# Kernel optimization log

Measured on AMD Instinct MI355X. Metric: run time of the kernel, lower is better.

Reference implementation:

```python
import jax, jax.numpy as jnp
import numpy as np

PAD = 4  # kernel 9, 'same' padding

def _conv1d(x, w):
    # x: [B, C, L], w: [O, I, K] -> [B, O, L] (same padding)
    return jax.lax.conv_general_dilated(x, w, (1,), [(PAD, PAD)],
                                        dimension_numbers=("NCW", "OIW", "NCW"))

def _sweep(x, w, b, axis, reverse):
    # Sequential SCNN sweep along `axis`: slice_i = relu(conv1d(slice_i) + b + slice_{i-1})
    xs = jnp.moveaxis(x, axis, 0)  # [L, B, C, K_len]
    if reverse:
        xs = xs[::-1]
    def step(carry, row):
        y = jax.nn.relu(_conv1d(row, w) + b[None, :, None] + carry)
        return y, y
    _, outs = jax.lax.scan(step, xs[0], xs[1:])
    res = jnp.concatenate([xs[:1], outs], axis=0)
    if reverse:
        res = res[::-1]
    return jnp.moveaxis(res, 0, axis)

def setup_inputs() -> dict:
    key = jax.random.key(0)
    ks = jax.random.split(key, 9)
    B, C, H, W, K = 16, 64, 128, 256, 9
    scale = 1.0 / np.sqrt(C * K).astype(np.float32)
    inp = {"x": jax.random.normal(ks[0], (B, C, H, W), jnp.float32)}
    for i, n in enumerate(["ud", "du", "lr", "rl"]):
        inp[f"w_{n}"] = jax.random.normal(ks[1 + 2 * i], (C, C, K), jnp.float32) * scale
        inp[f"b_{n}"] = jax.random.normal(ks[2 + 2 * i], (C,), jnp.float32) * scale
    return inp

def reference(x, w_ud, b_ud, w_du, b_du, w_lr, b_lr, w_rl, b_rl):
    # down sweep over rows (conv along width), then up sweep
    x = _sweep(x, w_ud, b_ud, axis=2, reverse=False)
    x = _sweep(x, w_du, b_du, axis=2, reverse=True)
    # left->right sweep over columns (conv along height), then right->left
    x = _sweep(x, w_lr, b_lr, axis=3, reverse=False)
    x = _sweep(x, w_rl, b_rl, axis=3, reverse=True)
    return x
```

## Files before the change

kernel.cpp:

```cpp
#include <hip/hip_runtime.h>

#define B_ 16
#define C_ 64
#define H_ 128
#define W_ 256
#define K_ 9
#define KDIM_ (K_*C_)

typedef __attribute__((ext_vector_type(8))) short short8_t;
typedef __attribute__((ext_vector_type(4))) float f32x4;

static __device__ __forceinline__ float bf2f(unsigned short u) {
  union { unsigned int i; float f; } v; v.i = ((unsigned int)u) << 16; return v.f;
}
static __device__ __forceinline__ unsigned short f2bf(float f) {
  union { float f; unsigned int i; } v; v.f = f;
  unsigned int r = v.i + 0x7FFF + ((v.i >> 16) & 1);
  return (unsigned short)(r >> 16);
}

static __device__ __forceinline__ void gload_lds16(const void* g, void* l) {
  __builtin_amdgcn_global_load_lds(
      (const __attribute__((address_space(1))) unsigned int*)g,
      (__attribute__((address_space(3))) unsigned int*)l, 16, 0, 0);
}

__global__ __launch_bounds__(256) void prep_w_all(const float* __restrict__ w0,
                                                  const float* __restrict__ w1,
                                                  const float* __restrict__ w2,
                                                  const float* __restrict__ w3,
                                                  unsigned short* __restrict__ A2,
                                                  float* __restrict__ ZPf) {
  if (blockIdx.y == 0 && blockIdx.x == 0) ZPf[threadIdx.x] = 0.f;
  int idx = blockIdx.x * 256 + threadIdx.x;
  if (idx >= C_ * KDIM_) return;
  int which = blockIdx.y;
  const float* w = (which == 0) ? w0 : (which == 1) ? w1 : (which == 2) ? w2 : w3;
  unsigned short* out = A2 + (size_t)which * (C_ * KDIM_);
  int co = idx / KDIM_, k = idx % KDIM_;
  int ci = k & 63, kk = k >> 6;
  out[((size_t)(k >> 3) * 64 + co) * 8 + (k & 7)] =
      f2bf(w[((size_t)co * C_ + ci) * K_ + kk]);
}

__global__ __launch_bounds__(256) void transpose_in(const float* __restrict__ x,
                                                    unsigned short* __restrict__ Xt) {
  __shared__ float tile[64][65];
  const int w0 = blockIdx.x * 64, h = blockIdx.y, b = blockIdx.z;
  const int t = threadIdx.x;
#pragma unroll
  for (int rep = 0; rep < 16; ++rep) {
    int idx = rep * 256 + t;
    int ci = idx >> 6, wl = idx & 63;
    tile[ci][wl] = x[((size_t)(b * C_ + ci) * H_ + h) * W_ + w0 + wl];
  }
  __syncthreads();
#pragma unroll
  for (int rep = 0; rep < 8; ++rep) {
    int idx = rep * 256 + t;
    int wl = idx >> 5, cp = idx & 31;
    unsigned v = (unsigned)f2bf(tile[cp*2][wl]) | ((unsigned)f2bf(tile[cp*2+1][wl]) << 16);
    *(unsigned*)(Xt + ((size_t)(b * H_ + h) * W_ + w0 + wl) * C_ + cp * 2) = v;
  }
}

__global__ __launch_bounds__(256) void transpose_out_wh(const unsigned short* __restrict__ F,
                                                        float* __restrict__ out) {
  __shared__ float tile[64][65];
  const int w0 = blockIdx.x * 64, h = blockIdx.y, b = blockIdx.z;
  const int t = threadIdx.x;
#pragma unroll
  for (int rep = 0; rep < 4; ++rep) {
    int idx = rep * 256 + t;
    int cp = idx & 15, wl = idx >> 4;
    uint2 v = *(const uint2*)(F + ((size_t)(b * W_ + w0 + wl) * H_ + h) * C_ + cp * 4);
    tile[wl][cp*4+0] = bf2f((unsigned short)v.x);
    tile[wl][cp*4+1] = bf2f((unsigned short)(v.x >> 16));
    tile[wl][cp*4+2] = bf2f((unsigned short)v.y);
    tile[wl][cp*4+3] = bf2f((unsigned short)(v.y >> 16));
  }
  __syncthreads();
#pragma unroll
  for (int rep = 0; rep < 16; ++rep) {
    int idx = rep * 256 + t;
    int ci = idx >> 6, wl = idx & 63;
    out[((size_t)(b * C_ + ci) * H_ + h) * W_ + w0 + wl] = tile[wl][ci];
  }
}

template<int QLEN>
__global__ __launch_bounds__(256, 1) void conv7(const unsigned short* __restrict__ X,
                                                unsigned short* __restrict__ Y,
                                                const unsigned short* __restrict__ A2,
                                                const float* __restrict__ bias,
                                                const unsigned short* __restrict__ ZP) {
  constexpr int SEGROWS = 256 / QLEN;
  constexpr int NG      = (256 + 8 * SEGROWS) / 8;
  __shared__ __align__(16) char lds[73728 + 2 * 34816];
  char* Alds  = lds;
  char* xbuf0 = lds + 73728;
  char* xbuf1 = lds + 73728 + 34816;

  const int t = threadIdx.x;
  const int lane = t & 63, wv = t >> 6;
  const int llo = lane & 15, lhi = lane >> 4;

#pragma unroll
  for (int i = 0; i < 18; ++i) {
    int m = wv + i * 4;
    gload_lds16(A2 + (size_t)m * 512 + lane * 8, Alds + m * 1024);
  }

  auto stageX = [&](char* dst, int u) {
#pragma unroll
    for (int i = 0; i < 9; ++i) {
      int gl = wv + i * 4;
      if (gl < NG) {
        int strip = (SEGROWS == 2 && gl >= 17) ? 1 : 0;
        int gg = gl - strip * 17;
        int r = gg * 8 + (lane >> 3);
        int slot = lane & 7;
        int chunk = slot ^ (r & 7);
        int q = r - 4;
        int rowId = (SEGROWS == 1) ? u : u * 2 + strip;
        const void* src = ((unsigned)q < (unsigned)QLEN)
            ? (const void*)(X + (size_t)rowId * (QLEN * 64) + (size_t)q * 64 + chunk * 8)
            : (const void*)(ZP + slot * 8);
        gload_lds16(src, dst + strip * 17408 + gg * 1024);
      }
    }
  };

  float4 bv[4];
#pragma unroll
  for (int j = 0; j < 4; ++j) bv[j] = *(const float4*)(bias + j * 16 + lhi * 4);

  const int stripoff = (SEGROWS == 1) ? 0 : (wv >> 1) * 17408;
  const int posbase  = (SEGROWS == 1) ? wv * 64 : (wv & 1) * 64;

  const int u0 = blockIdx.x * 8;
  stageX(xbuf0, u0);
  __syncthreads();

  for (int tt = 0; tt < 8; ++tt) {
    const int u = u0 + tt;
    char* cur = (tt & 1) ? xbuf1 : xbuf0;
    char* nxt = (tt & 1) ? xbuf0 : xbuf1;
    if (tt < 7) stageX(nxt, u + 1);

    const char* xb = cur + stripoff;
    f32x4 acc[4][4];
#pragma unroll
    for (int i = 0; i < 4; ++i)
#pragma unroll
      for (int j = 0; j < 4; ++j) { f32x4 z = {0.f,0.f,0.f,0.f}; acc[i][j] = z; }

#pragma unroll
    for (int step = 0; step < 18; ++step) {
      const int kk = step >> 1;
      const int cg = (step & 1) * 4 + lhi;
      short8_t a[4], f[4];
#pragma unroll
      for (int j = 0; j < 4; ++j)
        a[j] = *(const short8_t*)(Alds + step * 4096 + lhi * 1024 + j * 256 + llo * 16);
#pragma unroll
      for (int i = 0; i < 4; ++i) {
        int r = posbase + i * 16 + llo + kk;
        f[i] = *(const short8_t*)(xb + r * 128 + ((cg ^ (r & 7)) << 4));
      }
#pragma unroll
      for (int i = 0; i < 4; ++i)
#pragma unroll
        for (int j = 0; j < 4; ++j)
          acc[i][j] = __builtin_amdgcn_mfma_f32_16x16x32_bf16(a[j], f[i], acc[i][j], 0, 0, 0);
    }

    const int outRow = (SEGROWS == 1) ? u : u * 2 + (wv >> 1);
    const size_t rowbase = (size_t)outRow * (QLEN * 64);
#pragma unroll
    for (int j = 0; j < 4; ++j) {
#pragma unroll
      for (int i = 0; i < 4; ++i) {
        const int q = posbase + i * 16 + llo;
        float v0 = acc[i][j][0] + bv[j].x;
        float v1 = acc[i][j][1] + bv[j].y;
        float v2 = acc[i][j][2] + bv[j].z;
        float v3 = acc[i][j][3] + bv[j].w;
        unsigned lo, hi;
        asm("v_cvt_pk_bf16_f32 %0, %1, %2" : "=v"(lo) : "v"(v0), "v"(v1));
        asm("v_cvt_pk_bf16_f32 %0, %1, %2" : "=v"(hi) : "v"(v2), "v"(v3));
        uint2 ov; ov.x = lo; ov.y = hi;
        *(uint2*)(Y + rowbase + (size_t)q * 64 + j * 16 + lhi * 4) = ov;
      }
    }
    if (tt < 7) {
      asm volatile("s_waitcnt vmcnt(16)\n\ts_barrier" ::: "memory");
    }
  }
}

template<int PLEN, int QLEN, int REV, int TRANS>
__global__ __launch_bounds__(128) void scan_o4(unsigned short* __restrict__ conv,
                                               const unsigned short* __restrict__ prev,
                                               unsigned short* __restrict__ outT) {
  int idx = blockIdx.x * 128 + threadIdx.x;
  int cq = idx & 15;
  int q  = (idx >> 4) % QLEN;
  int b  = idx / (16 * QLEN);
  const ptrdiff_t dp = (REV ? -1 : 1) * (ptrdiff_t)(QLEN * 64);
  const int p0 = REV ? PLEN - 1 : 0;
  size_t off = ((size_t)(b * PLEN + p0) * QLEN + q) * 64 + cq * 4;
  size_t offT = 0; ptrdiff_t dpT = 0;
  if (TRANS) {
    offT = ((size_t)(b * QLEN + q) * PLEN + p0) * 64 + cq * 4;
    dpT = (REV ? -1 : 1) * (ptrdiff_t)64;
  }
  uint2 pv = *(const uint2*)(prev + off);
  if (TRANS) *(uint2*)(outT + offT) = pv; else *(uint2*)(conv + off) = pv;
  float y0 = bf2f((unsigned short)pv.x), y1 = bf2f((unsigned short)(pv.x >> 16));
  float y2 = bf2f((unsigned short)pv.y), y3 = bf2f((unsigned short)(pv.y >> 16));
  uint2 c[16];
#pragma unroll
  for (int j = 0; j < 16; ++j) c[j] = *(const uint2*)(conv + off + (ptrdiff_t)(j + 1) * dp);
  for (int base = 1; base < PLEN; base += 16) {
#pragma unroll
    for (int j = 0; j < 16; ++j) {
      int s = base + j;
      if (s < PLEN) {
        off += dp;
        if (TRANS) offT += dpT;
        y0 = fmaxf(bf2f((unsigned short)c[j].x) + y0, 0.f);
        y1 = fmaxf(bf2f((unsigned short)(c[j].x >> 16)) + y1, 0.f);
        y2 = fmaxf(bf2f((unsigned short)c[j].y) + y2, 0.f);
        y3 = fmaxf(bf2f((unsigned short)(c[j].y >> 16)) + y3, 0.f);
        uint2 ov;
        ov.x = (unsigned)f2bf(y0) | ((unsigned)f2bf(y1) << 16);
        ov.y = (unsigned)f2bf(y2) | ((unsigned)f2bf(y3) << 16);
        if (TRANS) *(uint2*)(outT + offT) = ov; else *(uint2*)(conv + off) = ov;
        if (s + 16 < PLEN) c[j] = *(const uint2*)(conv + off + 16 * dp);
      }
    }
  }
}

template<int PLEN, int QLEN, int REV>
__global__ __launch_bounds__(128) void scan_o2(unsigned short* __restrict__ conv,
                                               const unsigned short* __restrict__ prev) {
  int idx = blockIdx.x * 128 + threadIdx.x;
  int cp = idx & 31;
  int q  = (idx >> 5) % QLEN;
  int b  = idx / (32 * QLEN);
  const ptrdiff_t dp = (REV ? -1 : 1) * (ptrdiff_t)(QLEN * 64);
  const int p0 = REV ? PLEN - 1 : 0;
  size_t off = ((size_t)(b * PLEN + p0) * QLEN + q) * 64 + cp * 2;
  unsigned pv = *(const unsigned*)(prev + off);
  *(unsigned*)(conv + off) = pv;
  float y0 = bf2f((unsigned short)pv), y1 = bf2f((unsigned short)(pv >> 16));
  unsigned c[16];
#pragma unroll
  for (int j = 0; j < 16; ++j) c[j] = *(const unsigned*)(conv + off + (ptrdiff_t)(j + 1) * dp);
  for (int base = 1; base < PLEN; base += 16) {
#pragma unroll
    for (int j = 0; j < 16; ++j) {
      int s = base + j;
      if (s < PLEN) {
        off += dp;
        y0 = fmaxf(bf2f((unsigned short)c[j]) + y0, 0.f);
        y1 = fmaxf(bf2f((unsigned short)(c[j] >> 16)) + y1, 0.f);
        *(unsigned*)(conv + off) = (unsigned)f2bf(y0) | ((unsigned)f2bf(y1) << 16);
        if (s + 16 < PLEN) c[j] = *(const unsigned*)(conv + off + 16 * dp);
      }
    }
  }
}

extern "C" void kernel_launch(void* const* d_in, const int* in_sizes, int n_in,
                              void* d_out, int out_size, void* d_ws, size_t ws_size,
                              hipStream_t stream) {
  const float* x    = (const float*)d_in[0];
  const float* w_ud = (const float*)d_in[1];
  const float* b_ud = (const float*)d_in[2];
  const float* w_du = (const float*)d_in[3];
  const float* b_du = (const float*)d_in[4];
  const float* w_lr = (const float*)d_in[5];
  const float* b_lr = (const float*)d_in[6];
  const float* w_rl = (const float*)d_in[7];
  const float* b_rl = (const float*)d_in[8];

  unsigned short* A  = (unsigned short*)d_ws;
  unsigned short* Bb = (unsigned short*)((char*)d_ws + 67108864);
  unsigned short* Cc = (unsigned short*)((char*)d_ws + 134217728);
  unsigned short* A2 = (unsigned short*)((char*)d_ws + 201326592);
  unsigned short* ZP = (unsigned short*)((char*)d_ws + 202375168);
  unsigned short* A2_ud = A2 + 0 * (C_ * KDIM_);
  unsigned short* A2_du = A2 + 1 * (C_ * KDIM_);
  unsigned short* A2_lr = A2 + 2 * (C_ * KDIM_);
  unsigned short* A2_rl = A2 + 3 * (C_ * KDIM_);

  dim3 pg((C_ * KDIM_ + 255) / 256, 4);
  prep_w_all<<<pg, 256, 0, stream>>>(w_ud, w_du, w_lr, w_rl, A2, (float*)ZP);

  transpose_in<<<dim3(4, H_, B_), 256, 0, stream>>>(x, A);

  conv7<W_><<<256, 256, 0, stream>>>(A, Bb, A2_ud, b_ud, ZP);
  scan_o4<H_, W_, 0, 0><<<512, 128, 0, stream>>>(Bb, A, nullptr);

  conv7<W_><<<256, 256, 0, stream>>>(Bb, Cc, A2_du, b_du, ZP);
  scan_o4<H_, W_, 1, 1><<<512, 128, 0, stream>>>(Cc, Bb, A);

  conv7<H_><<<256, 256, 0, stream>>>(A, Bb, A2_lr, b_lr, ZP);
  scan_o2<W_, H_, 0><<<512, 128, 0, stream>>>(Bb, A);

  conv7<H_><<<256, 256, 0, stream>>>(Bb, Cc, A2_rl, b_rl, ZP);
  scan_o2<W_, H_, 1><<<512, 128, 0, stream>>>(Cc, Bb);

  transpose_out_wh<<<dim3(4, H_, B_), 256, 0, stream>>>(Cc, (float*)d_out);
}
```

Measured before the change: 356.4 us.

## Fuse final right-to-left scan with output transpose to fp32 NCHW

Replaces the last scan kernel and the separate transpose-out kernel with one kernel. The fused kernel runs the sequential scan along width, stages the results in a swizzled LDS tile and writes fp32 NCHW output in chunks of 64 columns. This removes one full bf16 write and re-read of the intermediate tensor plus one kernel launch. In exchange the grid is smaller (512 blocks of 128 threads with 4 rows each), each chunk flush adds block-wide syncs, and the flush loop issues scalar stores.

```diff
diff --git a/kernel.cpp b/kernel.cpp
--- a/kernel.cpp
+++ b/kernel.cpp
@@ -64,30 +64,6 @@
   }
 }
 
-__global__ __launch_bounds__(256) void transpose_out_wh(const unsigned short* __restrict__ F,
-                                                        float* __restrict__ out) {
-  __shared__ float tile[64][65];
-  const int w0 = blockIdx.x * 64, h = blockIdx.y, b = blockIdx.z;
-  const int t = threadIdx.x;
-#pragma unroll
-  for (int rep = 0; rep < 4; ++rep) {
-    int idx = rep * 256 + t;
-    int cp = idx & 15, wl = idx >> 4;
-    uint2 v = *(const uint2*)(F + ((size_t)(b * W_ + w0 + wl) * H_ + h) * C_ + cp * 4);
-    tile[wl][cp*4+0] = bf2f((unsigned short)v.x);
-    tile[wl][cp*4+1] = bf2f((unsigned short)(v.x >> 16));
-    tile[wl][cp*4+2] = bf2f((unsigned short)v.y);
-    tile[wl][cp*4+3] = bf2f((unsigned short)(v.y >> 16));
-  }
-  __syncthreads();
-#pragma unroll
-  for (int rep = 0; rep < 16; ++rep) {
-    int idx = rep * 256 + t;
-    int ci = idx >> 6, wl = idx & 63;
-    out[((size_t)(b * C_ + ci) * H_ + h) * W_ + w0 + wl] = tile[wl][ci];
-  }
-}
-
 template<int QLEN>
 __global__ __launch_bounds__(256, 1) void conv7(const unsigned short* __restrict__ X,
                                                 unsigned short* __restrict__ Y,
@@ -274,6 +250,58 @@
   }
 }
 
+__global__ __launch_bounds__(128) void scan4t(const unsigned short* __restrict__ conv,
+                                              const unsigned short* __restrict__ prev,
+                                              float* __restrict__ out) {
+  __shared__ unsigned tile[64 * 128];
+  const int t = threadIdx.x;
+  const int cp = t & 31, hh = t >> 5;
+  const int hg = blockIdx.x, b = blockIdx.y;
+  const int h = hg * 4 + hh;
+  const int wvid = t >> 6, wl = t & 63;
+
+  const ptrdiff_t dp = -(ptrdiff_t)(H_ * 64);
+  size_t off = ((size_t)(b * W_ + (W_ - 1)) * H_ + h) * 64 + cp * 2;
+
+  auto flushChunk = [&](int w0) {
+    __syncthreads();
+    for (int p = 0; p < 64; ++p) {
+      int combo = p * 2 + wvid;
+      int fh = combo >> 5, fcp = combo & 31;
+      unsigned v = tile[wl * 128 + fh * 32 + (fcp ^ (wl & 31))];
+      size_t ob = ((size_t)(b * C_ + fcp * 2) * H_ + hg * 4 + fh) * W_ + w0 + wl;
+      out[ob] = bf2f((unsigned short)v);
+      out[ob + (size_t)H_ * W_] = bf2f((unsigned short)(v >> 16));
+    }
+    __syncthreads();
+  };
+
+  unsigned pv = *(const unsigned*)(prev + off);
+  float y0 = bf2f((unsigned short)pv), y1 = bf2f((unsigned short)(pv >> 16));
+  tile[63 * 128 + hh * 32 + (cp ^ 31)] = pv;
+
+  unsigned c[16];
+#pragma unroll
+  for (int j = 0; j < 16; ++j)
+    c[j] = *(const unsigned*)(conv + off + (ptrdiff_t)(j + 1) * dp);
+
+  for (int base = 1; base < W_; base += 16) {
+#pragma unroll
+    for (int j = 0; j < 16; ++j) {
+      int s = base + j;
+      off += dp;
+      unsigned cv = c[j];
+      y0 = fmaxf(bf2f((unsigned short)cv) + y0, 0.f);
+      y1 = fmaxf(bf2f((unsigned short)(cv >> 16)) + y1, 0.f);
+      int w = W_ - 1 - s;
+      tile[(w & 63) * 128 + hh * 32 + (cp ^ (w & 31))] =
+          (unsigned)f2bf(y0) | ((unsigned)f2bf(y1) << 16);
+      if (s + 16 < W_) c[j] = *(const unsigned*)(conv + off + 16 * dp);
+      if ((s & 63) == 63) flushChunk(w);
+    }
+  }
+}
+
 extern "C" void kernel_launch(void* const* d_in, const int* in_sizes, int n_in,
                               void* d_out, int out_size, void* d_ws, size_t ws_size,
                               hipStream_t stream) {
@@ -312,7 +340,5 @@
   scan_o2<W_, H_, 0><<<512, 128, 0, stream>>>(Bb, A);
 
   conv7<H_><<<256, 256, 0, stream>>>(Bb, Cc, A2_rl, b_rl, ZP);
-  scan_o2<W_, H_, 1><<<512, 128, 0, stream>>>(Cc, Bb);
-
-  transpose_out_wh<<<dim3(4, H_, B_), 256, 0, stream>>>(Cc, (float*)d_out);
-}
+  scan4t<<<dim3(32, B_), 128, 0, stream>>>(Cc, Bb, (float*)d_out);
+}
```

Result: no change. 357.6 us (+0.3%).
